# Performance work log

Measured on AMD Instinct MI355X. Metric: run time of the kernel, lower is better.

## Reference

```python
import jax, jax.numpy as jnp
import numpy as np

B, C, IC, H, W = 4, 256, 128, 64, 64
EPS = 1e-5  # BatchNorm eps (eval mode, running stats)


def conv_bn(x, w, b, gamma, beta, mean, var, relu):
    # 1x1 conv == channel contraction; BN in eval mode (affine w/ running stats)
    y = jnp.einsum('oc,bchw->bohw', w, x) + b[None, :, None, None]
    scale = gamma * jax.lax.rsqrt(var + EPS)
    shift = beta - mean * scale
    y = y * scale[None, :, None, None] + shift[None, :, None, None]
    return jax.nn.relu(y) if relu else y


def setup_inputs() -> dict:
    key = jax.random.key(0)
    ks = jax.random.split(key, 32)

    def branch(i, co, ci):
        return dict(
            w=jax.random.normal(ks[i], (co, ci), jnp.float32) * 0.05,
            b=jax.random.normal(ks[i + 1], (co,), jnp.float32) * 0.05,
            gamma=jax.random.uniform(ks[i + 2], (co,), jnp.float32, 0.5, 1.5),
            beta=jax.random.normal(ks[i + 3], (co,), jnp.float32) * 0.05,
            mean=jax.random.normal(ks[i + 4], (co,), jnp.float32) * 0.05,
            var=jax.random.uniform(ks[i + 5], (co,), jnp.float32, 0.5, 1.5),
        )

    g = branch(0, IC, C)
    th = branch(6, IC, C)
    ph = branch(12, IC, C)
    wo = branch(18, C, IC)
    inp = {'x': jax.random.normal(ks[24], (B, C, H, W), jnp.float32)}
    for pre, p in (('g', g), ('th', th), ('ph', ph), ('w', wo)):
        for k, v in p.items():
            inp[f'{pre}_{k}'] = v
    return inp


def reference(x, g_w, g_b, g_gamma, g_beta, g_mean, g_var,
              th_w, th_b, th_gamma, th_beta, th_mean, th_var,
              ph_w, ph_b, ph_gamma, ph_beta, ph_mean, ph_var,
              w_w, w_b, w_gamma, w_beta, w_mean, w_var):
    b, c, h, w = x.shape
    ic = g_w.shape[0]
    g_x = conv_bn(x, g_w, g_b, g_gamma, g_beta, g_mean, g_var, True).reshape(b, ic, h * w)     # [b,ic,n]
    theta = conv_bn(x, th_w, th_b, th_gamma, th_beta, th_mean, th_var, True).reshape(b, ic, h * w)
    phi = conv_bn(x, ph_w, ph_b, ph_gamma, ph_beta, ph_mean, ph_var, True).reshape(b, ic, h * w)
    # unscaled attention over flattened spatial positions
    f = jnp.einsum('bcn,bcm->bnm', theta, phi)     # [b,n,n]
    a = jax.nn.softmax(f, axis=2)
    y = jnp.einsum('bnm,bcm->bcn', a, g_x)         # [b,ic,n]
    y = y.reshape(b, ic, h, w)
    y = conv_bn(y, w_w, w_b, w_gamma, w_beta, w_mean, w_var, False)
    return y + x
```

## Files before the change

### kernel.cpp

```cpp
#include <hip/hip_runtime.h>
#include <math.h>

typedef __attribute__((ext_vector_type(8))) short short8;
typedef __attribute__((ext_vector_type(8))) _Float16 half8;
typedef __attribute__((ext_vector_type(4))) float f32x4;

#define NSP 4096
#define CIN 256
#define ICH 128
#define SPLITS 4
#define TILES_PER_SPLIT 16
#define LOG2E 1.44269504088896f

__device__ __forceinline__ unsigned short f2h(float x){
  union { _Float16 h; unsigned short u; } v; v.h = (_Float16)x; return v.u;
}
__device__ __forceinline__ float h2f(unsigned short u){
  union { _Float16 h; unsigned short u; } v; v.u = u; return (float)v.h;
}
__device__ __forceinline__ unsigned pk2h(float a, float b){
  union { __fp16 __attribute__((ext_vector_type(2))) v; unsigned u; } r;
  r.v = __builtin_amdgcn_cvt_pkrtz(a, b);
  return r.u;
}
__device__ __forceinline__ float fexp2(float x){
  float r;
  asm("v_exp_f32 %0, %1" : "=v"(r) : "v"(x));
  return r;
}
__device__ __forceinline__ int swz(int row, int e){ return e ^ ((row & 7) << 3); }

__device__ __forceinline__ f32x4 mfmah(short8 a, short8 b, f32x4 c){
  union { short8 s; half8 h; } ua, ub; ua.s = a; ub.s = b;
  return __builtin_amdgcn_mfma_f32_16x16x32_f16(ua.h, ub.h, c, 0, 0, 0);
}

__device__ __forceinline__ void st4h(unsigned short* p, unsigned short a, unsigned short b,
                                     unsigned short c, unsigned short d){
  ushort4 v; v.x=a; v.y=b; v.z=c; v.w=d;
  *(ushort4*)p = v;
}

__device__ __forceinline__ void gload_lds16(const unsigned short* g, unsigned short* l){
  __builtin_amdgcn_global_load_lds(
      (const __attribute__((address_space(1))) unsigned int*)g,
      (__attribute__((address_space(3))) unsigned int*)l, 16, 0, 0);
}

__device__ __forceinline__ void stage_nc(const unsigned short* gbase, unsigned short* lds,
                                         int w, int l){
  #pragma unroll
  for (int i=0;i<4;++i){
    int rl = 16*w + 4*i + (l>>4);
    int eg = ((l&15)*8) ^ ((rl&7)<<3);
    gload_lds16(gbase + (size_t)rl*128 + eg, lds + w*2048 + i*512);
  }
}

__device__ __forceinline__ int kperm(int q){
  return ((q>>4)&1)*4 + ((q>>2)&3)*8 + (q&3);
}

__global__ __launch_bounds__(256) void conv_fused_k(
    const float* __restrict__ x,
    const float* __restrict__ w0, const float* __restrict__ b0,
    const float* __restrict__ ga0, const float* __restrict__ be0,
    const float* __restrict__ me0, const float* __restrict__ va0,
    const float* __restrict__ w1, const float* __restrict__ b1,
    const float* __restrict__ ga1, const float* __restrict__ be1,
    const float* __restrict__ me1, const float* __restrict__ va1,
    const float* __restrict__ w2, const float* __restrict__ b2,
    const float* __restrict__ ga2, const float* __restrict__ be2,
    const float* __restrict__ me2, const float* __restrict__ va2,
    unsigned short* __restrict__ outg, unsigned short* __restrict__ outt,
    unsigned short* __restrict__ outp)
{
  const int b = blockIdx.z, nt = blockIdx.x, ot = blockIdx.y;
  const int n0 = nt*64, o0 = ot*64;
  const int t = threadIdx.x, w = t>>6, l = t&63;
  __shared__ unsigned short xs[64][64];
  __shared__ unsigned short ws[3][64][64];
  __shared__ float sc_s[3][64], sh_s[3][64];
  if (t < 64){
    int o = o0 + t;
    float s0 = ga0[o]*rsqrtf(va0[o]+1e-5f);
    sc_s[0][t]=s0; sh_s[0][t]=be0[o]-me0[o]*s0+b0[o]*s0;
    float s1 = ga1[o]*rsqrtf(va1[o]+1e-5f);
    sc_s[1][t]=s1*LOG2E; sh_s[1][t]=(be1[o]-me1[o]*s1+b1[o]*s1)*LOG2E;
    float s2 = ga2[o]*rsqrtf(va2[o]+1e-5f);
    sc_s[2][t]=s2; sh_s[2][t]=be2[o]-me2[o]*s2+b2[o]*s2;
  }
  const f32x4 Z = {0.f,0.f,0.f,0.f};
  f32x4 acc[3][4];
  #pragma unroll
  for (int br=0;br<3;++br) for (int i=0;i<4;++i) acc[br][i] = Z;
  const float* Wt[3] = {w0, w1, w2};

  for (int kc = 0; kc < CIN; kc += 64){
    __syncthreads();
    #pragma unroll
    for (int p = 0; p < 4; ++p){
      int cw = p*16 + (t>>4);
      int q4 = (t&15)*4;
      float4 xv = *(const float4*)(x + ((size_t)b*CIN + kc + cw)*NSP + n0 + q4);
      float xa[4] = {xv.x, xv.y, xv.z, xv.w};
      #pragma unroll
      for (int i=0;i<4;++i){
        int r = q4 + i;
        xs[r][swz(r, cw)] = f2h(xa[i]);
      }
      #pragma unroll
      for (int br=0;br<3;++br){
        float4 wv = *(const float4*)(Wt[br] + (size_t)(o0 + cw)*CIN + kc + q4);
        int cs = swz(cw, q4);
        st4h(&ws[br][cw][cs], f2h(wv.x), f2h(wv.y), f2h(wv.z), f2h(wv.w));
      }
    }
    __syncthreads();
    #pragma unroll
    for (int kf = 0; kf < 2; ++kf){
      int ko = kf*32 + (l>>4)*8;
      int wr = 16*w + (l&15);
      short8 wf0 = *(const short8*)&ws[0][wr][swz(wr, ko)];
      short8 wf1 = *(const short8*)&ws[1][wr][swz(wr, ko)];
      short8 wf2 = *(const short8*)&ws[2][wr][swz(wr, ko)];
      #pragma unroll
      for (int nf = 0; nf < 4; ++nf){
        int xr = 16*nf + (l&15);
        short8 xf = *(const short8*)&xs[xr][swz(xr, ko)];
        acc[0][nf] = mfmah(wf0, xf, acc[0][nf]);
        acc[1][nf] = mfmah(xf, wf1, acc[1][nf]);
        acc[2][nf] = mfmah(xf, wf2, acc[2][nf]);
      }
    }
  }
  #pragma unroll
  for (int j=0;j<4;++j){
    int ol = 16*w + (l>>4)*4 + j;
    float s = sc_s[0][ol], sh = sh_s[0][ol];
    #pragma unroll
    for (int nf=0;nf<4;++nf){
      int n = n0 + 16*nf + (l&15);
      int nst = (n & ~31) | kperm(n & 31);
      float v = fmaxf(acc[0][nf][j]*s + sh, 0.f);
      outg[((size_t)b*ICH + o0 + ol)*NSP + nst] = f2h(v);
    }
  }
  {
    int ol = 16*w + (l&15);
    float s1 = sc_s[1][ol], sh1 = sh_s[1][ol];
    float s2 = sc_s[2][ol], sh2 = sh_s[2][ol];
    #pragma unroll
    for (int nf=0; nf<4; ++nf)
      #pragma unroll
      for (int j=0;j<4;++j){
        int n = n0 + 16*nf + (l>>4)*4 + j;
        float v1 = fmaxf(acc[1][nf][j]*s1 + sh1, 0.f);
        float v2 = fmaxf(acc[2][nf][j]*s2 + sh2, 0.f);
        outt[((size_t)b*NSP + n)*ICH + o0 + ol] = f2h(v1);
        outp[((size_t)b*NSP + n)*ICH + o0 + ol] = f2h(v2);
      }
  }
}

__global__ __launch_bounds__(256, 2) void attn_k(
  const unsigned short* __restrict__ thp, const unsigned short* __restrict__ php,
  const unsigned short* __restrict__ gb, unsigned short* __restrict__ ypart,
  float* __restrict__ ml)
{
  const int bx = blockIdx.x;
  const int xcd = bx & 7, jj = bx >> 3;
  const int combo = xcd*2 + (jj>>5);
  const int qt = jj & 31;
  const int b = combo & 3, s = combo >> 2;
  const int n0 = qt*128;
  const int t = threadIdx.x, w = t>>6, l = t&63;

  __shared__ unsigned short kb[2][64][128];
  __shared__ unsigned short vb[2][128][64];

  stage_nc(thp + ((size_t)b*NSP + n0      )*ICH, &kb[0][0][0], w, l);
  stage_nc(thp + ((size_t)b*NSP + n0 + 64 )*ICH, &kb[1][0][0], w, l);
  __syncthreads();
  short8 qf0[4], qf1[4];
  {
    int qr = 16*w + (l&15);
    #pragma unroll
    for (int kf=0;kf<4;++kf){
      int ko = kf*32 + (l>>4)*8;
      qf0[kf] = *(const short8*)&kb[0][qr][swz(qr, ko)];
      qf1[kf] = *(const short8*)&kb[1][qr][swz(qr, ko)];
    }
  }
  __syncthreads();

  const f32x4 Z = {0.f,0.f,0.f,0.f};
  f32x4 oa0[8], oa1[8];
  #pragma unroll
  for (int i=0;i<8;++i){ oa0[i]=Z; oa1[i]=Z; }
  float m0r = -1e30f, m1r = -1e30f;
  float l0r = 0.f, l1r = 0.f;
  unsigned pk0[8], pk1[8];

  const int tile0 = s*TILES_PER_SPLIT;

  const unsigned short* kp[4];
  const unsigned short* vp[4];
  {
    const unsigned short* kbase = php + ((size_t)b*NSP + tile0*64)*ICH;
    const unsigned short* vbase = gb + (size_t)b*ICH*NSP + tile0*64;
    #pragma unroll
    for (int i=0;i<4;++i){
      int rl = 16*w + 4*i + (l>>4);
      int eg = ((l&15)*8) ^ ((rl&7)<<3);
      kp[i] = kbase + (size_t)rl*128 + eg;
      int cl = 32*w + 8*i + (l>>3);
      int me = ((l&7)*8) ^ ((cl&7)<<3);
      vp[i] = vbase + (size_t)cl*NSP + me;
    }
  }
  {
    unsigned short* kd = &kb[0][0][0] + w*2048;
    unsigned short* vd = &vb[0][0][0] + w*2048;
    #pragma unroll
    for (int i=0;i<4;++i){
      gload_lds16(kp[i], kd + i*512); kp[i] += 64*ICH;
      gload_lds16(vp[i], vd + i*512); vp[i] += 64;
    }
  }
  __syncthreads();
  int cur = 0;

  for (int it = 0; it < TILES_PER_SPLIT; ++it){
    if (it < TILES_PER_SPLIT-1){
      unsigned short* kd = &kb[cur^1][0][0] + w*2048;
      unsigned short* vd = &vb[cur^1][0][0] + w*2048;
      #pragma unroll
      for (int i=0;i<4;++i){
        gload_lds16(kp[i], kd + i*512); kp[i] += 64*ICH;
        gload_lds16(vp[i], vd + i*512); vp[i] += 64;
      }
    }

    f32x4 f0[4], f1[4];
    #pragma unroll
    for (int i=0;i<4;++i){ f0[i]=Z; f1[i]=Z; }
    __builtin_amdgcn_s_setprio(1);
    #pragma unroll
    for (int mf=0; mf<4; ++mf){
      int kr = 16*mf + (l&15);
      #pragma unroll
      for (int kf=0; kf<4; ++kf){
        short8 bh = *(const short8*)&kb[cur][kr][swz(kr, kf*32 + (l>>4)*8)];
        f0[mf] = mfmah(bh, qf0[kf], f0[mf]);
        f1[mf] = mfmah(bh, qf1[kf], f1[mf]);
      }
    }
    __builtin_amdgcn_s_setprio(0);

    #pragma unroll
    for (int h=0; h<2; ++h){
      f32x4* f = h ? f1 : f0;
      float& mr = h ? m1r : m0r;
      float& lr = h ? l1r : l0r;
      f32x4* oa = h ? oa1 : oa0;
      unsigned* pk = h ? pk1 : pk0;
      float a0 = fmaxf(fmaxf(f[0][0], f[0][1]), fmaxf(f[0][2], f[0][3]));
      float a1 = fmaxf(fmaxf(f[1][0], f[1][1]), fmaxf(f[1][2], f[1][3]));
      float a2 = fmaxf(fmaxf(f[2][0], f[2][1]), fmaxf(f[2][2], f[2][3]));
      float a3 = fmaxf(fmaxf(f[3][0], f[3][1]), fmaxf(f[3][2], f[3][3]));
      float mx = fmaxf(fmaxf(a0, a1), fmaxf(a2, a3));
      mx = fmaxf(mx, __shfl_xor(mx, 16));
      mx = fmaxf(mx, __shfl_xor(mx, 32));
      if (__any(mx - mr > 11.5f)){
        float mn = fmaxf(mr, mx);
        float al = fexp2(mr - mn);
        mr = mn; lr *= al;
        #pragma unroll
        for (int j=0;j<4;++j){
          float alj = __shfl(al, (l>>4)*4 + j);
          #pragma unroll
          for (int cf=0;cf<8;++cf) oa[cf][j] *= alj;
        }
      }
      float s0 = 0.f, s1 = 0.f, s2 = 0.f, s3 = 0.f;
      #pragma unroll
      for (int mf=0;mf<4;++mf){
        float p0 = fexp2(f[mf][0] - mr);
        float p1 = fexp2(f[mf][1] - mr);
        float p2 = fexp2(f[mf][2] - mr);
        float p3 = fexp2(f[mf][3] - mr);
        pk[2*mf+0] = pk2h(p0, p1);
        pk[2*mf+1] = pk2h(p2, p3);
        s0 += p0; s1 += p1; s2 += p2; s3 += p3;
      }
      lr += (s0 + s1) + (s2 + s3);
    }

    __builtin_amdgcn_s_setprio(1);
    {
      int g8 = (l>>4)*8;
      #pragma unroll
      for (int mk=0;mk<2;++mk){
        union { unsigned u[4]; short8 s8; } a0u, a1u;
        #pragma unroll
        for (int q=0;q<4;++q){ a0u.u[q] = pk0[4*mk+q]; a1u.u[q] = pk1[4*mk+q]; }
        #pragma unroll
        for (int cf=0;cf<8;++cf){
          int vr = 16*cf + (l&15);
          short8 bv = *(const short8*)&vb[cur][vr][swz(vr, mk*32 + g8)];
          oa0[cf] = mfmah(a0u.s8, bv, oa0[cf]);
          oa1[cf] = mfmah(a1u.s8, bv, oa1[cf]);
        }
      }
    }
    __builtin_amdgcn_s_setprio(0);

    __syncthreads();
    cur ^= 1;
  }

  #pragma unroll
  for (int h=0; h<2; ++h){
    float mr = h ? m1r : m0r;
    float lr = h ? l1r : l0r;
    f32x4* oa = h ? oa1 : oa0;
    lr += __shfl_xor(lr, 16);
    lr += __shfl_xor(lr, 32);
    float invl = 1.f / lr;
    #pragma unroll
    for (int j=0;j<4;++j){
      float inv = __shfl(invl, (l>>4)*4 + j);
      int n = n0 + h*64 + 16*w + (l>>4)*4 + j;
      #pragma unroll
      for (int cf=0;cf<8;++cf){
        int c = 16*cf + (l&15);
        ypart[(((size_t)s*4 + b)*NSP + n)*ICH + c] = f2h(oa[cf][j]*inv);
      }
    }
    if (l < 16){
      int n = n0 + h*64 + 16*w + l;
      ml[(((size_t)s*4 + b)*NSP + n)*2 + 0] = mr;
      ml[(((size_t)s*4 + b)*NSP + n)*2 + 1] = lr;
    }
  }
}

__global__ __launch_bounds__(256) void final_k2(
  const unsigned short* __restrict__ ypart, const float* __restrict__ ml,
  const float* __restrict__ x, const float* __restrict__ Wm,
  const float* __restrict__ bias, const float* __restrict__ gamma,
  const float* __restrict__ beta, const float* __restrict__ mean,
  const float* __restrict__ var, float* __restrict__ out)
{
  const int b = blockIdx.z, oth = blockIdx.y, nt = blockIdx.x;
  const int n0 = nt*64, obase = oth*128;
  const int t = threadIdx.x, w = t>>6, l = t&63;
  __shared__ unsigned short ys[64][128];
  __shared__ unsigned short w2s[64][128];
  __shared__ float wc[SPLITS][64];
  __shared__ float sc_s[128], sh_s[128];
  if (t < 128){
    int o = obase + t;
    float s = gamma[o]*rsqrtf(var[o]+1e-5f);
    sc_s[t]=s; sh_s[t]=beta[o]-mean[o]*s+bias[o]*s;
  } else if (t < 192){
    int r = t - 128, n = n0 + r;
    float mv[SPLITS], lv[SPLITS];
    #pragma unroll
    for (int s=0;s<SPLITS;++s){
      mv[s] = ml[(((size_t)s*4 + b)*NSP + n)*2 + 0];
      lv[s] = ml[(((size_t)s*4 + b)*NSP + n)*2 + 1];
    }
    float M = fmaxf(fmaxf(mv[0],mv[1]), fmaxf(mv[2],mv[3]));
    float wsum = 0.f, wv[SPLITS];
    #pragma unroll
    for (int s=0;s<SPLITS;++s){ wv[s] = lv[s]*exp2f(mv[s]-M); wsum += wv[s]; }
    float inv = 1.f/wsum;
    #pragma unroll
    for (int s=0;s<SPLITS;++s) wc[s][r] = wv[s]*inv;
  }
  __syncthreads();
  #pragma unroll
  for (int p=0;p<4;++p){
    int id = p*256 + t, r = id>>4, c8 = (id&15)*8;
    float accv[8] = {0,0,0,0,0,0,0,0};
    #pragma unroll
    for (int s=0;s<SPLITS;++s){
      short8 v = *(const short8*)(ypart + (((size_t)s*4 + b)*NSP + n0 + r)*ICH + c8);
      float wgt = wc[s][r];
      #pragma unroll
      for (int i=0;i<8;++i) accv[i] += wgt * h2f(((unsigned short*)&v)[i]);
    }
    unsigned short hv[8];
    #pragma unroll
    for (int i=0;i<8;++i) hv[i] = f2h(accv[i]);
    *(short8*)&ys[r][swz(r,c8)] = *(short8*)hv;
  }

  const f32x4 Z = {0.f,0.f,0.f,0.f};
  #pragma unroll
  for (int ot2 = 0; ot2 < 2; ++ot2){
    const int o0 = obase + ot2*64;
    #pragma unroll
    for (int p=0;p<4;++p){
      int id = p*256 + t, r = id>>4, c8 = (id&15)*8;
      float4 u0 = *(const float4*)(Wm + (size_t)(o0 + r)*ICH + c8);
      float4 u1 = *(const float4*)(Wm + (size_t)(o0 + r)*ICH + c8 + 4);
      unsigned short wh[8] = {f2h(u0.x),f2h(u0.y),f2h(u0.z),f2h(u0.w),
                              f2h(u1.x),f2h(u1.y),f2h(u1.z),f2h(u1.w)};
      *(short8*)&w2s[r][swz(r,c8)] = *(short8*)wh;
    }
    __syncthreads();
    f32x4 acc[4];
    #pragma unroll
    for (int i=0;i<4;++i) acc[i]=Z;
    #pragma unroll
    for (int kf=0;kf<4;++kf){
      int ko = kf*32 + (l>>4)*8;
      int wr = 16*w + (l&15);
      short8 a = *(const short8*)&w2s[wr][swz(wr,ko)];
      #pragma unroll
      for (int nf=0;nf<4;++nf){
        int yr = 16*nf + (l&15);
        short8 bb = *(const short8*)&ys[yr][swz(yr,ko)];
        acc[nf] = mfmah(a, bb, acc[nf]);
      }
    }
    #pragma unroll
    for (int j=0;j<4;++j){
      int ol = 16*w + (l>>4)*4 + j;
      float s = sc_s[ot2*64 + ol], sh = sh_s[ot2*64 + ol];
      #pragma unroll
      for (int nf=0;nf<4;++nf){
        int n = n0 + 16*nf + (l&15);
        size_t idx = ((size_t)b*CIN + o0 + ol)*NSP + n;
        out[idx] = acc[nf][j]*s + sh + x[idx];
      }
    }
    __syncthreads();
  }
}

extern "C" void kernel_launch(void* const* d_in, const int* in_sizes, int n_in,
                              void* d_out, int out_size, void* d_ws, size_t ws_size,
                              hipStream_t stream){
  const float* x    = (const float*)d_in[0];
  const float* g_w  = (const float*)d_in[1];
  const float* g_b  = (const float*)d_in[2];
  const float* g_ga = (const float*)d_in[3];
  const float* g_be = (const float*)d_in[4];
  const float* g_me = (const float*)d_in[5];
  const float* g_va = (const float*)d_in[6];
  const float* t_w  = (const float*)d_in[7];
  const float* t_b  = (const float*)d_in[8];
  const float* t_ga = (const float*)d_in[9];
  const float* t_be = (const float*)d_in[10];
  const float* t_me = (const float*)d_in[11];
  const float* t_va = (const float*)d_in[12];
  const float* p_w  = (const float*)d_in[13];
  const float* p_b  = (const float*)d_in[14];
  const float* p_ga = (const float*)d_in[15];
  const float* p_be = (const float*)d_in[16];
  const float* p_me = (const float*)d_in[17];
  const float* p_va = (const float*)d_in[18];
  const float* w_w  = (const float*)d_in[19];
  const float* w_b  = (const float*)d_in[20];
  const float* w_ga = (const float*)d_in[21];
  const float* w_be = (const float*)d_in[22];
  const float* w_me = (const float*)d_in[23];
  const float* w_va = (const float*)d_in[24];

  char* ws = (char*)d_ws;
  const size_t SEG = (size_t)4*NSP*ICH*sizeof(unsigned short);
  unsigned short* th_t  = (unsigned short*)(ws);
  unsigned short* ph_t  = (unsigned short*)(ws + SEG);
  unsigned short* g_cn  = (unsigned short*)(ws + 2*SEG);
  unsigned short* ypart = (unsigned short*)(ws + 3*SEG);
  float*          mlb   = (float*)(ws + 3*SEG + SPLITS*SEG);

  dim3 blk(256,1,1);
  conv_fused_k<<<dim3(64,2,4), blk, 0, stream>>>(
      x,
      g_w, g_b, g_ga, g_be, g_me, g_va,
      t_w, t_b, t_ga, t_be, t_me, t_va,
      p_w, p_b, p_ga, p_be, p_me, p_va,
      g_cn, th_t, ph_t);
  attn_k<<<dim3(512,1,1), blk, 0, stream>>>(th_t, ph_t, g_cn, ypart, mlb);
  final_k2<<<dim3(64,2,4), blk, 0, stream>>>(ypart, mlb, x, w_w, w_b, w_ga, w_be, w_me, w_va, (float*)d_out);
}
```

Baseline: 69.89 us.

## Switch attention kernel to 32x32x16 MFMA tiles with 16-row swizzle

```diff
diff --git a/kernel.cpp b/kernel.cpp
--- a/kernel.cpp
+++ b/kernel.cpp
@@ -4,6 +4,7 @@
 typedef __attribute__((ext_vector_type(8))) short short8;
 typedef __attribute__((ext_vector_type(8))) _Float16 half8;
 typedef __attribute__((ext_vector_type(4))) float f32x4;
+typedef __attribute__((ext_vector_type(16))) float f32x16;
 
 #define NSP 4096
 #define CIN 256
@@ -29,10 +30,15 @@
   return r;
 }
 __device__ __forceinline__ int swz(int row, int e){ return e ^ ((row & 7) << 3); }
+__device__ __forceinline__ int swzK(int row, int e){ return e ^ ((row & 15) << 3); }
 
 __device__ __forceinline__ f32x4 mfmah(short8 a, short8 b, f32x4 c){
   union { short8 s; half8 h; } ua, ub; ua.s = a; ub.s = b;
   return __builtin_amdgcn_mfma_f32_16x16x32_f16(ua.h, ub.h, c, 0, 0, 0);
+}
+__device__ __forceinline__ f32x16 mfma32(short8 a, short8 b, f32x16 c){
+  union { short8 s; half8 h; } ua, ub; ua.s = a; ub.s = b;
+  return __builtin_amdgcn_mfma_f32_32x32x16_f16(ua.h, ub.h, c, 0, 0, 0);
 }
 
 __device__ __forceinline__ void st4h(unsigned short* p, unsigned short a, unsigned short b,
@@ -52,13 +58,14 @@
   #pragma unroll
   for (int i=0;i<4;++i){
     int rl = 16*w + 4*i + (l>>4);
-    int eg = ((l&15)*8) ^ ((rl&7)<<3);
+    int eg = ((l&15)*8) ^ ((rl&15)<<3);
     gload_lds16(gbase + (size_t)rl*128 + eg, lds + w*2048 + i*512);
   }
 }
 
 __device__ __forceinline__ int kperm(int q){
-  return ((q>>4)&1)*4 + ((q>>2)&3)*8 + (q&3);
+  int m = q & 15;
+  return (q & 16) | (((m>>2)&1)<<3) | (m&3) | (((m>>3)&1)<<2);
 }
 
 __global__ __launch_bounds__(256) void conv_fused_k(
@@ -175,32 +182,31 @@
   const int b = combo & 3, s = combo >> 2;
   const int n0 = qt*128;
   const int t = threadIdx.x, w = t>>6, l = t&63;
-
-  __shared__ unsigned short kb[2][64][128];
-  __shared__ unsigned short vb[2][128][64];
-
-  stage_nc(thp + ((size_t)b*NSP + n0      )*ICH, &kb[0][0][0], w, l);
-  stage_nc(thp + ((size_t)b*NSP + n0 + 64 )*ICH, &kb[1][0][0], w, l);
+  const int hi = l>>5, ln = l&31;
+
+  __shared__ unsigned short kb[2][8192];
+  __shared__ unsigned short vb[2][8192];
+
+  stage_nc(thp + ((size_t)b*NSP + n0      )*ICH, &kb[0][0], w, l);
+  stage_nc(thp + ((size_t)b*NSP + n0 + 64 )*ICH, &kb[1][0], w, l);
   __syncthreads();
-  short8 qf0[4], qf1[4];
+  short8 qf[8];
   {
-    int qr = 16*w + (l&15);
-    #pragma unroll
-    for (int kf=0;kf<4;++kf){
-      int ko = kf*32 + (l>>4)*8;
-      qf0[kf] = *(const short8*)&kb[0][qr][swz(qr, ko)];
-      qf1[kf] = *(const short8*)&kb[1][qr][swz(qr, ko)];
-    }
+    const unsigned short* qsrc = (w >> 1) ? &kb[1][0] : &kb[0][0];
+    int r = 32*(w & 1) + ln;
+    #pragma unroll
+    for (int kc=0;kc<8;++kc)
+      qf[kc] = *(const short8*)&qsrc[r*128 + swzK(r, kc*16 + 8*hi)];
   }
   __syncthreads();
 
-  const f32x4 Z = {0.f,0.f,0.f,0.f};
-  f32x4 oa0[8], oa1[8];
-  #pragma unroll
-  for (int i=0;i<8;++i){ oa0[i]=Z; oa1[i]=Z; }
-  float m0r = -1e30f, m1r = -1e30f;
-  float l0r = 0.f, l1r = 0.f;
-  unsigned pk0[8], pk1[8];
+  f32x16 oa[4];
+  #pragma unroll
+  for (int i=0;i<4;++i)
+    #pragma unroll
+    for (int j=0;j<16;++j) oa[i][j] = 0.f;
+  float mr = -1e30f, lr = 0.f;
+  unsigned pk[16];
 
   const int tile0 = s*TILES_PER_SPLIT;
 
@@ -212,7 +218,7 @@
     #pragma unroll
     for (int i=0;i<4;++i){
       int rl = 16*w + 4*i + (l>>4);
-      int eg = ((l&15)*8) ^ ((rl&7)<<3);
+      int eg = ((l&15)*8) ^ ((rl&15)<<3);
       kp[i] = kbase + (size_t)rl*128 + eg;
       int cl = 32*w + 8*i + (l>>3);
       int me = ((l&7)*8) ^ ((cl&7)<<3);
@@ -220,8 +226,8 @@
     }
   }
   {
-    unsigned short* kd = &kb[0][0][0] + w*2048;
-    unsigned short* vd = &vb[0][0][0] + w*2048;
+    unsigned short* kd = &kb[0][0] + w*2048;
+    unsigned short* vd = &vb[0][0] + w*2048;
     #pragma unroll
     for (int i=0;i<4;++i){
       gload_lds16(kp[i], kd + i*512); kp[i] += 64*ICH;
@@ -233,8 +239,8 @@
 
   for (int it = 0; it < TILES_PER_SPLIT; ++it){
     if (it < TILES_PER_SPLIT-1){
-      unsigned short* kd = &kb[cur^1][0][0] + w*2048;
-      unsigned short* vd = &vb[cur^1][0][0] + w*2048;
+      unsigned short* kd = &kb[cur^1][0] + w*2048;
+      unsigned short* vd = &vb[cur^1][0] + w*2048;
       #pragma unroll
       for (int i=0;i<4;++i){
         gload_lds16(kp[i], kd + i*512); kp[i] += 64*ICH;
@@ -242,107 +248,108 @@
       }
     }
 
-    f32x4 f0[4], f1[4];
-    #pragma unroll
-    for (int i=0;i<4;++i){ f0[i]=Z; f1[i]=Z; }
+    f32x16 sc0, sc1;
+    #pragma unroll
+    for (int j=0;j<16;++j){ sc0[j]=0.f; sc1[j]=0.f; }
     __builtin_amdgcn_s_setprio(1);
     #pragma unroll
-    for (int mf=0; mf<4; ++mf){
-      int kr = 16*mf + (l&15);
-      #pragma unroll
-      for (int kf=0; kf<4; ++kf){
-        short8 bh = *(const short8*)&kb[cur][kr][swz(kr, kf*32 + (l>>4)*8)];
-        f0[mf] = mfmah(bh, qf0[kf], f0[mf]);
-        f1[mf] = mfmah(bh, qf1[kf], f1[mf]);
-      }
+    for (int kc=0;kc<8;++kc){
+      int eo = kc*16 + 8*hi;
+      short8 a0 = *(const short8*)&kb[cur][(ln     )*128 + swzK(ln,      eo)];
+      short8 a1 = *(const short8*)&kb[cur][(32 + ln)*128 + swzK(32 + ln, eo)];
+      sc0 = mfma32(a0, qf[kc], sc0);
+      sc1 = mfma32(a1, qf[kc], sc1);
     }
     __builtin_amdgcn_s_setprio(0);
 
-    #pragma unroll
-    for (int h=0; h<2; ++h){
-      f32x4* f = h ? f1 : f0;
-      float& mr = h ? m1r : m0r;
-      float& lr = h ? l1r : l0r;
-      f32x4* oa = h ? oa1 : oa0;
-      unsigned* pk = h ? pk1 : pk0;
-      float a0 = fmaxf(fmaxf(f[0][0], f[0][1]), fmaxf(f[0][2], f[0][3]));
-      float a1 = fmaxf(fmaxf(f[1][0], f[1][1]), fmaxf(f[1][2], f[1][3]));
-      float a2 = fmaxf(fmaxf(f[2][0], f[2][1]), fmaxf(f[2][2], f[2][3]));
-      float a3 = fmaxf(fmaxf(f[3][0], f[3][1]), fmaxf(f[3][2], f[3][3]));
-      float mx = fmaxf(fmaxf(a0, a1), fmaxf(a2, a3));
-      mx = fmaxf(mx, __shfl_xor(mx, 16));
+    {
+      float t0 = fmaxf(fmaxf(sc0[0],sc0[1]),  fmaxf(sc0[2],sc0[3]));
+      float t1 = fmaxf(fmaxf(sc0[4],sc0[5]),  fmaxf(sc0[6],sc0[7]));
+      float t2 = fmaxf(fmaxf(sc0[8],sc0[9]),  fmaxf(sc0[10],sc0[11]));
+      float t3 = fmaxf(fmaxf(sc0[12],sc0[13]),fmaxf(sc0[14],sc0[15]));
+      float t4 = fmaxf(fmaxf(sc1[0],sc1[1]),  fmaxf(sc1[2],sc1[3]));
+      float t5 = fmaxf(fmaxf(sc1[4],sc1[5]),  fmaxf(sc1[6],sc1[7]));
+      float t6 = fmaxf(fmaxf(sc1[8],sc1[9]),  fmaxf(sc1[10],sc1[11]));
+      float t7 = fmaxf(fmaxf(sc1[12],sc1[13]),fmaxf(sc1[14],sc1[15]));
+      float mx = fmaxf(fmaxf(fmaxf(t0,t1),fmaxf(t2,t3)),
+                       fmaxf(fmaxf(t4,t5),fmaxf(t6,t7)));
       mx = fmaxf(mx, __shfl_xor(mx, 32));
       if (__any(mx - mr > 11.5f)){
         float mn = fmaxf(mr, mx);
         float al = fexp2(mr - mn);
         mr = mn; lr *= al;
         #pragma unroll
-        for (int j=0;j<4;++j){
-          float alj = __shfl(al, (l>>4)*4 + j);
+        for (int j=0;j<16;++j){
+          int rowj = (j&3) + 8*(j>>2) + 4*hi;
+          float alj = __shfl(al, rowj);
           #pragma unroll
-          for (int cf=0;cf<8;++cf) oa[cf][j] *= alj;
+          for (int ct=0;ct<4;++ct) oa[ct][j] *= alj;
         }
       }
-      float s0 = 0.f, s1 = 0.f, s2 = 0.f, s3 = 0.f;
-      #pragma unroll
-      for (int mf=0;mf<4;++mf){
-        float p0 = fexp2(f[mf][0] - mr);
-        float p1 = fexp2(f[mf][1] - mr);
-        float p2 = fexp2(f[mf][2] - mr);
-        float p3 = fexp2(f[mf][3] - mr);
-        pk[2*mf+0] = pk2h(p0, p1);
-        pk[2*mf+1] = pk2h(p2, p3);
-        s0 += p0; s1 += p1; s2 += p2; s3 += p3;
-      }
-      lr += (s0 + s1) + (s2 + s3);
+      float sA=0.f, sB=0.f, sC=0.f, sD=0.f;
+      #pragma unroll
+      for (int r=0;r<16;r+=4){
+        sc0[r]   = fexp2(sc0[r]  -mr); sA += sc0[r];
+        sc0[r+1] = fexp2(sc0[r+1]-mr); sB += sc0[r+1];
+        sc0[r+2] = fexp2(sc0[r+2]-mr); sC += sc0[r+2];
+        sc0[r+3] = fexp2(sc0[r+3]-mr); sD += sc0[r+3];
+      }
+      #pragma unroll
+      for (int r=0;r<16;r+=4){
+        sc1[r]   = fexp2(sc1[r]  -mr); sA += sc1[r];
+        sc1[r+1] = fexp2(sc1[r+1]-mr); sB += sc1[r+1];
+        sc1[r+2] = fexp2(sc1[r+2]-mr); sC += sc1[r+2];
+        sc1[r+3] = fexp2(sc1[r+3]-mr); sD += sc1[r+3];
+      }
+      lr += (sA + sB) + (sC + sD);
+      #pragma unroll
+      for (int s2=0;s2<2;++s2)
+        #pragma unroll
+        for (int q=0;q<4;++q){
+          pk[s2*4+q]   = pk2h(sc0[8*s2+2*q], sc0[8*s2+2*q+1]);
+          pk[8+s2*4+q] = pk2h(sc1[8*s2+2*q], sc1[8*s2+2*q+1]);
+        }
     }
 
     __builtin_amdgcn_s_setprio(1);
-    {
-      int g8 = (l>>4)*8;
-      #pragma unroll
-      for (int mk=0;mk<2;++mk){
-        union { unsigned u[4]; short8 s8; } a0u, a1u;
+    #pragma unroll
+    for (int mt=0;mt<2;++mt)
+      #pragma unroll
+      for (int s2=0;s2<2;++s2){
+        union { unsigned u[4]; short8 s8; } au;
         #pragma unroll
-        for (int q=0;q<4;++q){ a0u.u[q] = pk0[4*mk+q]; a1u.u[q] = pk1[4*mk+q]; }
+        for (int q=0;q<4;++q) au.u[q] = pk[8*mt+4*s2+q];
+        int eo = 32*mt + 16*s2 + 8*hi;
         #pragma unroll
-        for (int cf=0;cf<8;++cf){
-          int vr = 16*cf + (l&15);
-          short8 bv = *(const short8*)&vb[cur][vr][swz(vr, mk*32 + g8)];
-          oa0[cf] = mfmah(a0u.s8, bv, oa0[cf]);
-          oa1[cf] = mfmah(a1u.s8, bv, oa1[cf]);
+        for (int ct=0;ct<4;++ct){
+          int cr = 32*ct + ln;
+          short8 bv = *(const short8*)&vb[cur][cr*64 + swz(cr, eo)];
+          oa[ct] = mfma32(au.s8, bv, oa[ct]);
         }
       }
-    }
     __builtin_amdgcn_s_setprio(0);
 
     __syncthreads();
     cur ^= 1;
   }
 
-  #pragma unroll
-  for (int h=0; h<2; ++h){
-    float mr = h ? m1r : m0r;
-    float lr = h ? l1r : l0r;
-    f32x4* oa = h ? oa1 : oa0;
-    lr += __shfl_xor(lr, 16);
-    lr += __shfl_xor(lr, 32);
-    float invl = 1.f / lr;
-    #pragma unroll
-    for (int j=0;j<4;++j){
-      float inv = __shfl(invl, (l>>4)*4 + j);
-      int n = n0 + h*64 + 16*w + (l>>4)*4 + j;
-      #pragma unroll
-      for (int cf=0;cf<8;++cf){
-        int c = 16*cf + (l&15);
-        ypart[(((size_t)s*4 + b)*NSP + n)*ICH + c] = f2h(oa[cf][j]*inv);
-      }
-    }
-    if (l < 16){
-      int n = n0 + h*64 + 16*w + l;
-      ml[(((size_t)s*4 + b)*NSP + n)*2 + 0] = mr;
-      ml[(((size_t)s*4 + b)*NSP + n)*2 + 1] = lr;
-    }
+  lr += __shfl_xor(lr, 32);
+  float invl = 1.f / lr;
+  #pragma unroll
+  for (int j=0;j<16;++j){
+    int rowj = (j&3) + 8*(j>>2) + 4*hi;
+    float invj = __shfl(invl, rowj);
+    int n = n0 + 32*w + rowj;
+    #pragma unroll
+    for (int ct=0;ct<4;++ct){
+      int c = 32*ct + ln;
+      ypart[(((size_t)s*4 + b)*NSP + n)*ICH + c] = f2h(oa[ct][j]*invj);
+    }
+  }
+  if (l < 32){
+    int n = n0 + 32*w + l;
+    ml[(((size_t)s*4 + b)*NSP + n)*2 + 0] = mr;
+    ml[(((size_t)s*4 + b)*NSP + n)*2 + 1] = lr;
   }
 }
 
```

Result: no change. 70.32 us (+0.6%).
